# Optimization experiments

Hardware: AMD Instinct MI355X
Metric: run time of the kernel (lower is better)

The kernel has to match this reference:

```python
import jax, jax.numpy as jnp
import numpy as np

N = 20000   # nodes per type per hop
E = 200000  # edges per relation per hop
H = 512     # node_feature_hid_len
FU = 512    # raw user feature len
FI = 256    # raw item feature len
NUM_RES = 2
NUM_DNN = 2


def setup_inputs() -> dict:
    key = jax.random.key(0)
    ks = iter(jax.random.split(key, 64))
    p = lambda shape: jax.random.normal(next(ks), shape, dtype=jnp.float32) * 0.05
    inp = {}
    # features per hop per type
    for h in range(3):
        inp[f'feat_user_h{h}'] = jax.random.normal(next(ks), (N, FU), dtype=jnp.float32)
        inp[f'feat_item_h{h}'] = jax.random.normal(next(ks), (N, FI), dtype=jnp.float32)
    del inp['feat_user_h2_']; 


def _unused():
    pass

# rebuild setup_inputs cleanly (above stub replaced)

def setup_inputs() -> dict:
    key = jax.random.key(0)
    ks = iter(jax.random.split(key, 64))
    p = lambda shape: jax.random.normal(next(ks), shape, dtype=jnp.float32) * 0.05
    inp = {}
    for h in range(3):
        inp[f'feat_user_h{h}'] = jax.random.normal(next(ks), (N, FU), dtype=jnp.float32)
        inp[f'feat_item_h{h}'] = jax.random.normal(next(ks), (N, FI), dtype=jnp.float32)
    for name in ('edges_UI_h0', 'edges_IU_h0', 'edges_UI_h1', 'edges_IU_h1'):
        inp[name] = jax.random.randint(next(ks), (2, E), 0, N, dtype=jnp.int32)
    # per-node-type input transforms
    inp['W_user'] = p((FU, H)); inp['b_user'] = jnp.zeros((H,), jnp.float32)
    inp['W_item'] = p((FI, H)); inp['b_item'] = jnp.zeros((H,), jnp.float32)
    # per-relation GATConv params, stacked over 2 relations [UI, IU]
    inp['gat_feat_W'] = p((2, H, H)); inp['gat_feat_b'] = jnp.zeros((2, H), jnp.float32)
    inp['gat_att_w'] = p((2, 2 * H)); inp['gat_att_b'] = jnp.zeros((2,), jnp.float32)
    inp['gat_bias'] = jnp.zeros((2, H), jnp.float32)
    # Res_DNN params
    inp['prep_W'] = p((H, H)); inp['prep_b'] = jnp.zeros((H,), jnp.float32)
    inp['dnn_W'] = p((NUM_RES, NUM_DNN, H, H)); inp['dnn_b'] = jnp.zeros((NUM_RES, NUM_DNN, H), jnp.float32)
    inp['dnn_ln_g'] = jnp.ones((NUM_RES, NUM_DNN, H), jnp.float32); inp['dnn_ln_b'] = jnp.zeros((NUM_RES, NUM_DNN, H), jnp.float32)
    inp['res_ln_g'] = jnp.ones((NUM_RES, H), jnp.float32); inp['res_ln_b'] = jnp.zeros((NUM_RES, H), jnp.float32)
    inp['cls_W'] = p((H, 1)); inp['cls_b'] = jnp.zeros((1,), jnp.float32)
    return inp


def _ln(x, g, b, eps=1e-5):
    mu = jnp.mean(x, axis=-1, keepdims=True)
    var = jnp.mean((x - mu) ** 2, axis=-1, keepdims=True)
    return (x - mu) * jax.lax.rsqrt(var + eps) * g + b


def _gat(head_h, tail_h, edges, fW, fb, aw, ab, bias):
    # GATConv: feat_linear on both sides, tanh edge attention, per-source-row
    # sparse softmax, scatter-weighted sum of transformed tail features.
    s = head_h @ fW + fb            # [Nh, H]
    t = tail_h @ fW + fb            # [Nt, H]
    src, tgt = edges[0], edges[1]
    # att(cat([s_e, t_e])) split into per-node scores (same math as concat @ aw)
    e = jnp.tanh((s @ aw[:H])[src] + (t @ aw[H:])[tgt] + ab)  # [E]
    nh = head_h.shape[0]
    m = jax.ops.segment_max(e, src, num_segments=nh)
    ex = jnp.exp(e - m[src])
    den = jax.ops.segment_sum(ex, src, num_segments=nh)
    alpha = ex / den[src]
    hp = jax.ops.segment_sum(alpha[:, None] * t[tgt], src, num_segments=nh)
    return hp + bias


def _forward(feat_user_h0, feat_item_h0, feat_user_h1, feat_item_h1,
             feat_user_h2, feat_item_h2,
             W_user, b_user, W_item, b_item,
             gat_feat_W, gat_feat_b, gat_att_w, gat_att_b, gat_bias,
             prep_W, prep_b, dnn_W, dnn_b, dnn_ln_g, dnn_ln_b,
             res_ln_g, res_ln_b, cls_W, cls_b,
             edges_UI_h0, edges_IU_h0, edges_UI_h1, edges_IU_h1):
    def gat(r, head, tail, edges):
        return _gat(head, tail, edges, gat_feat_W[r], gat_feat_b[r],
                    gat_att_w[r], gat_att_b[r], gat_bias[r])
    # hop 2 (deepest): transformed source features
    su = feat_user_h2 @ W_user + b_user
    si = feat_item_h2 @ W_item + b_item
    # hop 1
    hu = feat_user_h1 @ W_user + b_user
    hi = feat_item_h1 @ W_item + b_item
    su_new = (hu + gat(0, hu, si, edges_UI_h1)) * 0.5  # mean of [self, UI agg]
    si_new = (hi + gat(1, hi, su, edges_IU_h1)) * 0.5
    su, si = su_new, si_new
    # hop 0
    hu = feat_user_h0 @ W_user + b_user
    hi = feat_item_h0 @ W_item + b_item
    su_new = (hu + gat(0, hu, si, edges_UI_h0)) * 0.5
    su = su_new  # target node type = 'user' (first key)
    # Res_DNN head
    x = su @ prep_W + prep_b
    for r in range(NUM_RES):
        sc = x
        for d in range(NUM_DNN):
            x = _ln(jnp.tanh(x @ dnn_W[r, d] + dnn_b[r, d]), dnn_ln_g[r, d], dnn_ln_b[r, d])
        x = _ln(jnp.tanh(sc + x), res_ln_g[r], res_ln_b[r])
    return jax.nn.sigmoid(x @ cls_W + cls_b)  # [N, 1]


def reference(feat_user_h0, feat_item_h0, feat_user_h1, feat_item_h1,
              feat_user_h2, feat_item_h2,
              edges_UI_h0, edges_IU_h0, edges_UI_h1, edges_IU_h1,
              W_user, b_user, W_item, b_item,
              gat_feat_W, gat_feat_b, gat_att_w, gat_att_b, gat_bias,
              prep_W, prep_b, dnn_W, dnn_b, dnn_ln_g, dnn_ln_b,
              res_ln_g, res_ln_b, cls_W, cls_b):
    return _forward(feat_user_h0, feat_item_h0, feat_user_h1, feat_item_h1,
                    feat_user_h2, feat_item_h2,
                    W_user, b_user, W_item, b_item,
                    gat_feat_W, gat_feat_b, gat_att_w, gat_att_b, gat_bias,
                    prep_W, prep_b, dnn_W, dnn_b, dnn_ln_g, dnn_ln_b,
                    res_ln_g, res_ln_b, cls_W, cls_b,
                    edges_UI_h0, edges_IU_h0, edges_UI_h1, edges_IU_h1)
```

## Files before the change

### kernel.cpp

```cpp
#include <hip/hip_runtime.h>
#include <math.h>

#define NN 20000
#define NE 200000
#define HH 512

typedef __attribute__((ext_vector_type(8))) short short8v;
typedef __attribute__((ext_vector_type(4))) float f32x4;

__device__ inline short f2bf(float f) {
    union { float f; unsigned u; } v; v.f = f;
    unsigned r = (v.u + 0x7fffu + ((v.u >> 16) & 1u)) >> 16;
    return (short)r;
}
__device__ inline float bf2f(short s) {
    union { unsigned u; float f; } v;
    v.u = ((unsigned)(unsigned short)s) << 16;
    return v.f;
}

__device__ inline void gload_lds16(const void* g, void* l) {
    __builtin_amdgcn_global_load_lds(
        (const __attribute__((address_space(1))) void*)g,
        (__attribute__((address_space(3))) void*)l, 16, 0, 0);
}

__global__ __launch_bounds__(256)
void wtr_all(const float* __restrict__ Wu, const float* __restrict__ Wi,
             const float* __restrict__ gfW, const float* __restrict__ prW,
             const float* __restrict__ dW,
             short* __restrict__ WTu, short* __restrict__ WTi,
             short* __restrict__ WTg0, short* __restrict__ WTg1,
             short* __restrict__ WTpr, short* __restrict__ WTd)
{
    __shared__ float t[32][33];
    int z = blockIdx.z;
    const float* src; short* dst; int K;
    if (z == 0)      { src = Wu;  dst = WTu;  K = 512; }
    else if (z == 1) { src = Wi;  dst = WTi;  K = 256; }
    else if (z == 2) { src = gfW; dst = WTg0; K = 512; }
    else if (z == 3) { src = gfW + (size_t)512 * 512; dst = WTg1; K = 512; }
    else if (z == 4) { src = prW; dst = WTpr; K = 512; }
    else { src = dW + (size_t)(z - 5) * 512 * 512;
           dst = WTd + (size_t)(z - 5) * 512 * 512; K = 512; }
    int by = blockIdx.y * 32;
    if (by >= K) return;
    int bx = blockIdx.x * 32;
    int tx = threadIdx.x, ty = threadIdx.y;
    for (int i = ty; i < 32; i += 8)
        t[i][tx] = src[(size_t)(by + i) * 512 + bx + tx];
    __syncthreads();
    for (int i = ty; i < 32; i += 8)
        dst[(size_t)(bx + i) * K + by + tx] = f2bf(t[tx][i]);
}

__global__ __launch_bounds__(256)
void mfma_lin(const short* __restrict__ X, const short* __restrict__ WT,
              const float* __restrict__ bias, float* __restrict__ outF,
              short* __restrict__ outB, int M, int K,
              const short* __restrict__ rdH, const short* __restrict__ rdT,
              const float* __restrict__ rduv, const float* __restrict__ rds0,
              float* __restrict__ rdss, float* __restrict__ rdts, int rdN)
{
    __shared__ short8v pool[4096];

    const int tid = threadIdx.x;
    const int lane = tid & 63;
    const int w = tid >> 6;

    const int nby = (M + 127) >> 7;
    const int nwg = nby << 2;
    int id = blockIdx.x;

    if (id >= nwg) {
        int row = (id - nwg) * 4 + w;
        if (row >= rdN) return;
        short8v h = ((const short8v*)(rdH + (size_t)row * HH))[lane];
        short8v t = ((const short8v*)(rdT + (size_t)row * HH))[lane];
        const float4* up = (const float4*)rduv + lane * 2;
        const float4* vp = (const float4*)(rduv + HH) + lane * 2;
        float4 u0 = up[0], u1 = up[1], v0 = vp[0], v1 = vp[1];
        float a = bf2f(h[0])*u0.x + bf2f(h[1])*u0.y + bf2f(h[2])*u0.z + bf2f(h[3])*u0.w
                + bf2f(h[4])*u1.x + bf2f(h[5])*u1.y + bf2f(h[6])*u1.z + bf2f(h[7])*u1.w;
        float b = bf2f(t[0])*v0.x + bf2f(t[1])*v0.y + bf2f(t[2])*v0.z + bf2f(t[3])*v0.w
                + bf2f(t[4])*v1.x + bf2f(t[5])*v1.y + bf2f(t[6])*v1.z + bf2f(t[7])*v1.w;
#pragma unroll
        for (int m = 32; m >= 1; m >>= 1) {
            a += __shfl_xor(a, m);
            b += __shfl_xor(b, m);
        }
        if (lane == 0) { rdss[row] = a + rds0[0]; rdts[row] = b + rds0[1]; }
        return;
    }

    const int q = nwg >> 3, r = nwg & 7;
    int xcd = id & 7, wi = id >> 3;
    int wgid = (xcd < r ? xcd * (q + 1) : r * (q + 1) + (xcd - r) * q) + wi;
    const int col0 = (wgid & 3) * 128;
    const int row0 = (wgid >> 2) * 128;

    const int wr = (w >> 1) * 64;
    const int wc = (w & 1) * 64;

    const short* gsrc[8];
#pragma unroll
    for (int g = 0; g < 8; ++g) {
        int p = w * 512 + g * 64 + lane;
        if (p < 1024) {
            int row = p >> 3;
            int c = (p & 7) ^ (row & 7);
            int ga = row0 + row; if (ga >= M) ga = M - 1;
            gsrc[g] = X + (size_t)ga * K + c * 8;
        } else {
            int qq = p - 1024;
            int col = qq >> 3;
            int c = (qq & 7) ^ (col & 7);
            gsrc[g] = WT + (size_t)(col0 + col) * K + c * 8;
        }
    }

    int ar[2][4], br[2][4];
#pragma unroll
    for (int kk = 0; kk < 2; ++kk) {
#pragma unroll
        for (int i = 0; i < 4; ++i) {
            int rr = wr + i * 16 + (lane & 15);
            ar[kk][i] = rr * 8 + ((kk * 4 + (lane >> 4)) ^ (rr & 7));
            int nn = wc + i * 16 + (lane & 15);
            br[kk][i] = 1024 + nn * 8 + ((kk * 4 + (lane >> 4)) ^ (nn & 7));
        }
    }

    f32x4 acc[4][4];
#pragma unroll
    for (int i = 0; i < 4; ++i)
#pragma unroll
        for (int j = 0; j < 4; ++j)
            acc[i][j] = (f32x4){0.f, 0.f, 0.f, 0.f};

    auto stage = [&](int buf, int kk) {
        short8v* base = pool + buf * 2048 + w * 512;
#pragma unroll
        for (int g = 0; g < 8; ++g)
            gload_lds16(gsrc[g] + kk, base + g * 64);
    };

    const int nt = K >> 6;
    stage(0, 0);
    if (nt > 1) stage(1, 64);
    int cur = 0;
    for (int t = 0; t < nt; ++t) {
        if (t + 1 < nt) asm volatile("s_waitcnt vmcnt(8)" ::: "memory");
        else            asm volatile("s_waitcnt vmcnt(0)" ::: "memory");
        __builtin_amdgcn_s_barrier();
        const short8v* S = pool + cur * 2048;
#pragma unroll
        for (int kk = 0; kk < 2; ++kk) {
            short8v af[4], bf[4];
#pragma unroll
            for (int i = 0; i < 4; ++i) af[i] = S[ar[kk][i]];
#pragma unroll
            for (int j = 0; j < 4; ++j) bf[j] = S[br[kk][j]];
#pragma unroll
            for (int i = 0; i < 4; ++i)
#pragma unroll
                for (int j = 0; j < 4; ++j)
                    acc[i][j] = __builtin_amdgcn_mfma_f32_16x16x32_bf16(af[i], bf[j], acc[i][j], 0, 0, 0);
        }
        __builtin_amdgcn_s_barrier();
        if (t + 2 < nt) stage(cur, (t + 2) * 64);
        cur ^= 1;
    }

    float bj[4];
#pragma unroll
    for (int j = 0; j < 4; ++j)
        bj[j] = bias[col0 + wc + j * 16 + (lane & 15)];

    if (outF) {
#pragma unroll
        for (int i = 0; i < 4; ++i) {
#pragma unroll
            for (int rr = 0; rr < 4; ++rr) {
                int row = row0 + wr + i * 16 + (lane >> 4) * 4 + rr;
                if (row < M) {
                    float* op = outF + (size_t)row * HH + col0 + wc + (lane & 15);
#pragma unroll
                    for (int j = 0; j < 4; ++j) op[j * 16] = acc[i][j][rr] + bj[j];
                }
            }
        }
    }
    if (outB) {
        short* lt = (short*)pool;
#pragma unroll
        for (int i = 0; i < 4; ++i)
#pragma unroll
            for (int rr = 0; rr < 4; ++rr) {
                int lrow = wr + i * 16 + (lane >> 4) * 4 + rr;
#pragma unroll
                for (int j = 0; j < 4; ++j)
                    lt[lrow * 136 + wc + j * 16 + (lane & 15)] = f2bf(acc[i][j][rr] + bj[j]);
            }
        __syncthreads();
#pragma unroll
        for (int k = 0; k < 8; ++k) {
            int row = (tid >> 4) + 16 * k;
            int seg = tid & 15;
            int grow = row0 + row;
            if (grow < M) {
                short8v vv = *(short8v*)(lt + row * 136 + seg * 8);
                *(short8v*)(outB + (size_t)grow * HH + col0 + seg * 8) = vv;
            }
        }
    }
}

__global__ __launch_bounds__(256)
void mfma_linf(const float* __restrict__ XA, const float* __restrict__ XB2,
               int NA, const short* __restrict__ WT,
               const float* __restrict__ bias, short* __restrict__ outB,
               int M, int K)
{
    __shared__ short8v pool[2304];

    const int tid = threadIdx.x;
    const int lane = tid & 63;
    const int w = tid >> 6;

    const int nby = (M + 127) >> 7;
    const int nwg = nby << 2;
    const int q = nwg >> 3, r = nwg & 7;
    int id = blockIdx.x;
    int xcd = id & 7, wi = id >> 3;
    int wgid = (xcd < r ? xcd * (q + 1) : r * (q + 1) + (xcd - r) * q) + wi;
    const int col0 = (wgid & 3) * 128;
    const int row0 = (wgid >> 2) * 128;

    const int wr = (w >> 1) * 64;
    const int wc = (w & 1) * 64;

    const int srow = tid >> 1;
    const int sc0 = (tid & 1) * 2;
    int garow = row0 + srow; if (garow >= M) garow = M - 1;
    const float* abase = ((garow < NA) ? XA + (size_t)garow * K
                                       : XB2 + (size_t)(garow - NA) * K) + sc0 * 8;
    const int aswz = (srow >> 1) & 3;
    const int wi0 = srow * 4 + (sc0 ^ aswz);
    const int wi1 = srow * 4 + ((sc0 + 1) ^ aswz);

    const short* bsrc0; const short* bsrc1;
    int bbase0, bbase1;
    {
        int p0 = w * 128 + lane;
        int col = p0 >> 2;
        int c = (p0 & 3) ^ ((col >> 1) & 3);
        bsrc0 = WT + (size_t)(col0 + col) * K + c * 8;
        bbase0 = w * 128;
        int p1 = w * 128 + 64 + lane;
        col = p1 >> 2;
        c = (p1 & 3) ^ ((col >> 1) & 3);
        bsrc1 = WT + (size_t)(col0 + col) * K + c * 8;
        bbase1 = w * 128 + 64;
    }

    int ar[4], br[4];
#pragma unroll
    for (int i = 0; i < 4; ++i) {
        int rr = wr + i * 16 + (lane & 15);
        ar[i] = rr * 4 + ((lane >> 4) ^ ((rr >> 1) & 3));
        int nn = wc + i * 16 + (lane & 15);
        br[i] = 512 + nn * 4 + ((lane >> 4) ^ ((nn >> 1) & 3));
    }

    f32x4 acc[4][4];
#pragma unroll
    for (int i = 0; i < 4; ++i)
#pragma unroll
        for (int j = 0; j < 4; ++j)
            acc[i][j] = (f32x4){0.f, 0.f, 0.f, 0.f};

    const int nt = K >> 5;
    float4 rA0[4], rA1[4];

#define ISSUE_A(RA, T) {                                                   \
        const float4* p_ = (const float4*)(abase + (T) * 32);              \
        RA[0] = p_[0]; RA[1] = p_[1]; RA[2] = p_[2]; RA[3] = p_[3]; }
#define ISSUE_B(BUF, T) {                                                  \
        short8v* bb_ = pool + (BUF) * 1024 + 512;                          \
        gload_lds16(bsrc0 + (T) * 32, bb_ + bbase0);                       \
        gload_lds16(bsrc1 + (T) * 32, bb_ + bbase1); }
#define LINF_BODY(BUF, RA, T) {                                            \
        short8v s0_, s1_;                                                  \
        s0_[0]=f2bf(RA[0].x); s0_[1]=f2bf(RA[0].y); s0_[2]=f2bf(RA[0].z); s0_[3]=f2bf(RA[0].w); \
        s0_[4]=f2bf(RA[1].x); s0_[5]=f2bf(RA[1].y); s0_[6]=f2bf(RA[1].z); s0_[7]=f2bf(RA[1].w); \
        s1_[0]=f2bf(RA[2].x); s1_[1]=f2bf(RA[2].y); s1_[2]=f2bf(RA[2].z); s1_[3]=f2bf(RA[2].w); \
        s1_[4]=f2bf(RA[3].x); s1_[5]=f2bf(RA[3].y); s1_[6]=f2bf(RA[3].z); s1_[7]=f2bf(RA[3].w); \
        short8v* A_ = pool + (BUF) * 1024;                                 \
        A_[wi0] = s0_; A_[wi1] = s1_;                                      \
        if ((T) + 1 < nt) asm volatile("s_waitcnt vmcnt(6) lgkmcnt(0)" ::: "memory"); \
        else              asm volatile("s_waitcnt vmcnt(0) lgkmcnt(0)" ::: "memory"); \
        __builtin_amdgcn_s_barrier();                                      \
        const short8v* S_ = pool + (BUF) * 1024;                           \
        short8v af_[4], bf_[4];                                            \
        _Pragma("unroll")                                                  \
        for (int i_ = 0; i_ < 4; ++i_) af_[i_] = S_[ar[i_]];               \
        _Pragma("unroll")                                                  \
        for (int j_ = 0; j_ < 4; ++j_) bf_[j_] = S_[br[j_]];               \
        _Pragma("unroll")                                                  \
        for (int i_ = 0; i_ < 4; ++i_)                                     \
            _Pragma("unroll")                                              \
            for (int j_ = 0; j_ < 4; ++j_)                                 \
                acc[i_][j_] = __builtin_amdgcn_mfma_f32_16x16x32_bf16(af_[i_], bf_[j_], acc[i_][j_], 0, 0, 0); \
        __builtin_amdgcn_s_barrier();                                      \
        if ((T) + 2 < nt) { ISSUE_A(RA, (T) + 2); ISSUE_B(BUF, (T) + 2); } }

    ISSUE_A(rA0, 0);
    ISSUE_B(0, 0);
    ISSUE_A(rA1, 1);
    ISSUE_B(1, 1);
    for (int t = 0; t < nt; t += 2) {
        LINF_BODY(0, rA0, t);
        LINF_BODY(1, rA1, t + 1);
    }
#undef ISSUE_A
#undef ISSUE_B
#undef LINF_BODY

    float bj[4];
#pragma unroll
    for (int j = 0; j < 4; ++j)
        bj[j] = bias[col0 + wc + j * 16 + (lane & 15)];

    short* lt = (short*)pool;
#pragma unroll
    for (int i = 0; i < 4; ++i)
#pragma unroll
        for (int rr = 0; rr < 4; ++rr) {
            int lrow = wr + i * 16 + (lane >> 4) * 4 + rr;
#pragma unroll
            for (int j = 0; j < 4; ++j)
                lt[lrow * 136 + wc + j * 16 + (lane & 15)] = f2bf(acc[i][j][rr] + bj[j]);
        }
    __syncthreads();
#pragma unroll
    for (int k = 0; k < 8; ++k) {
        int row = (tid >> 4) + 16 * k;
        int seg = tid & 15;
        int grow = row0 + row;
        if (grow < M) {
            short8v vv = *(short8v*)(lt + row * 136 + seg * 8);
            *(short8v*)(outB + (size_t)grow * HH + col0 + seg * 8) = vv;
        }
    }
}

__global__ __launch_bounds__(256)
void gat_pre2(const float* __restrict__ gfW, const float* __restrict__ gfb,
              const float* __restrict__ gaw, float* __restrict__ uvall,
              float* __restrict__ s0t0all)
{
    int rrel = blockIdx.y;
    const float* fW = gfW + (size_t)rrel * HH * HH;
    const float* fb = gfb + rrel * HH;
    const float* aw = gaw + (size_t)rrel * 2 * HH;
    float* uv = uvall + rrel * 1024;
    float* s0t0 = s0t0all + rrel * 4;
    int row = blockIdx.x * 4 + (threadIdx.x >> 6);
    int lane = threadIdx.x & 63;
    const float4* ah = (const float4*)aw;
    const float4* at = (const float4*)(aw + HH);
    const float4* fp;
    if (row < 512)       fp = (const float4*)(fW + (size_t)row * HH);
    else if (row == 512) fp = (const float4*)fb;
    else return;
    float du = 0.f, dv = 0.f;
#pragma unroll
    for (int l = 0; l < 2; ++l) {
        int idx = lane * 2 + l;
        float4 f = fp[idx], a = ah[idx], b = at[idx];
        du += f.x*a.x + f.y*a.y + f.z*a.z + f.w*a.w;
        dv += f.x*b.x + f.y*b.y + f.z*b.z + f.w*b.w;
    }
#pragma unroll
    for (int m = 32; m >= 1; m >>= 1) {
        du += __shfl_xor(du, m);
        dv += __shfl_xor(dv, m);
    }
    if (lane == 0) {
        if (row < 512) { uv[row] = du; uv[512 + row] = dv; }
        else           { s0t0[0] = du; s0t0[1] = dv; }
    }
}

__global__ __launch_bounds__(256)
void count2_kernel(const int* __restrict__ s0, const int* __restrict__ s1,
                   int* __restrict__ c0, int* __restrict__ c1, int E)
{
    int i = blockIdx.x * blockDim.x + threadIdx.x;
    if (i < E) atomicAdd(&c0[s0[i]], 1);
    else if (i < 2 * E) atomicAdd(&c1[s1[i - E]], 1);
}

__global__ __launch_bounds__(1024)
void scan2_kernel(const int* __restrict__ c0, const int* __restrict__ c1,
                  int* __restrict__ o0, int* __restrict__ o1,
                  int* __restrict__ u0, int* __restrict__ u1, int n)
{
    const int* counts = blockIdx.x ? c1 : c0;
    int* offs = blockIdx.x ? o1 : o0;
    int* curs = blockIdx.x ? u1 : u0;
    __shared__ int part[1024];
    const int tid = threadIdx.x;
    const int CH = (n + 1023) / 1024;
    const int base = tid * CH;
    int s = 0;
    for (int i = 0; i < CH; ++i) {
        int idx = base + i;
        if (idx < n) s += counts[idx];
    }
    part[tid] = s;
    __syncthreads();
    for (int d = 1; d < 1024; d <<= 1) {
        int v = 0;
        if (tid >= d) v = part[tid - d];
        __syncthreads();
        if (tid >= d) part[tid] += v;
        __syncthreads();
    }
    int run = (tid == 0) ? 0 : part[tid - 1];
    for (int i = 0; i < CH; ++i) {
        int idx = base + i;
        if (idx < n) { offs[idx] = run; curs[idx] = run; run += counts[idx]; }
    }
    if (tid == 1023) offs[n] = run;
}

__global__ __launch_bounds__(256)
void fill_kernel(const int* __restrict__ src, const int* __restrict__ tgt,
                 const float* __restrict__ ss, const float* __restrict__ ts,
                 const float* __restrict__ ab_ptr, int* __restrict__ cursor,
                 int* __restrict__ tvals, float* __restrict__ wv,
                 int* __restrict__ eidx, int E)
{
    int i = blockIdx.x * blockDim.x + threadIdx.x;
    if (i >= E) return;
    int s = src[i], t = tgt[i];
    int pos = atomicAdd(&cursor[s], 1);
    tvals[pos] = t;
    wv[pos] = expf(tanhf(ss[s] + ts[t] + ab_ptr[0]));
    eidx[pos] = i;
}

__global__ __launch_bounds__(256)
void gat_agg_kernel(const int* __restrict__ offs, const int* __restrict__ tvals,
                    const float* __restrict__ wv, const int* __restrict__ eidx,
                    const short* __restrict__ T, const short* __restrict__ head,
                    const float* __restrict__ gbias, short* __restrict__ out, int N)
{
    __shared__ int   slt[4][512];
    __shared__ float slw[4][512];
    int w = threadIdx.x >> 6;
    int lane = threadIdx.x & 63;
    int s = blockIdx.x * 4 + w;
    if (s >= N) return;
    const int beg = offs[s], end = offs[s + 1];
    int L = end - beg;
    if (L > 512) L = 512;

    if (L <= 64) {
        int e = 0x7fffffff, t = 0; float fw = 0.f;
        if (lane < L) { e = eidx[beg + lane]; t = tvals[beg + lane]; fw = wv[beg + lane]; }
        int r = 0;
        for (int k = 0; k < L; ++k)
            r += (__shfl(e, k) < e) ? 1 : 0;
        if (lane < L) { slt[w][r] = t; slw[w][r] = fw; }
    } else {
        for (int j = lane; j < L; j += 64) {
            int e = eidx[beg + j];
            int r = 0;
            for (int k = 0; k < L; ++k) r += (eidx[beg + k] < e) ? 1 : 0;
            slt[w][r] = tvals[beg + j]; slw[w][r] = wv[beg + j];
        }
    }
    asm volatile("s_waitcnt lgkmcnt(0)" ::: "memory");

    float a[8];
#pragma unroll
    for (int q = 0; q < 8; ++q) a[q] = 0.f;
    float den = 0.f;

    int j = 0;
    for (; j + 8 <= L; j += 8) {
        short8v v[8];
        float wgt[8];
#pragma unroll
        for (int u = 0; u < 8; ++u) {
            wgt[u] = slw[w][j + u];
            v[u] = ((const short8v*)(T + (size_t)slt[w][j + u] * HH))[lane];
        }
#pragma unroll
        for (int u = 0; u < 8; ++u) {
            den += wgt[u];
#pragma unroll
            for (int q = 0; q < 8; ++q) a[q] = fmaf(wgt[u], bf2f(v[u][q]), a[q]);
        }
    }
    for (; j + 4 <= L; j += 4) {
        short8v v[4];
        float wgt[4];
#pragma unroll
        for (int u = 0; u < 4; ++u) {
            wgt[u] = slw[w][j + u];
            v[u] = ((const short8v*)(T + (size_t)slt[w][j + u] * HH))[lane];
        }
#pragma unroll
        for (int u = 0; u < 4; ++u) {
            den += wgt[u];
#pragma unroll
            for (int q = 0; q < 8; ++q) a[q] = fmaf(wgt[u], bf2f(v[u][q]), a[q]);
        }
    }
    for (; j < L; ++j) {
        float fw = slw[w][j];
        short8v tv = ((const short8v*)(T + (size_t)slt[w][j] * HH))[lane];
        den += fw;
#pragma unroll
        for (int q = 0; q < 8; ++q) a[q] = fmaf(fw, bf2f(tv[q]), a[q]);
    }
    float inv = (den > 0.f) ? 1.f / den : 0.f;

    short8v h = ((const short8v*)(head + (size_t)s * HH))[lane];
    const float4* bp = (const float4*)gbias + lane * 2;
    float4 b0 = bp[0], b1 = bp[1];
    float bb[8] = {b0.x, b0.y, b0.z, b0.w, b1.x, b1.y, b1.z, b1.w};
    short8v o;
#pragma unroll
    for (int q = 0; q < 8; ++q)
        o[q] = f2bf((bf2f(h[q]) + a[q] * inv + bb[q]) * 0.5f);
    ((short8v*)(out + (size_t)s * HH))[lane] = o;
}

__global__ __launch_bounds__(256)
void tanh_ln_kernel(const short* __restrict__ Z,
                    const float* __restrict__ g, const float* __restrict__ bta,
                    short* __restrict__ outB, int N)
{
    int row = blockIdx.x * 4 + (threadIdx.x >> 6);
    int lane = threadIdx.x & 63;
    if (row >= N) return;
    short8v zv = ((const short8v*)(Z + (size_t)row * HH))[lane];
    float v[8];
    float sum = 0.f, sum2 = 0.f;
#pragma unroll
    for (int q = 0; q < 8; ++q) {
        float t = tanhf(bf2f(zv[q]));
        v[q] = t; sum += t; sum2 = fmaf(t, t, sum2);
    }
#pragma unroll
    for (int m = 32; m >= 1; m >>= 1) {
        sum += __shfl_xor(sum, m); sum2 += __shfl_xor(sum2, m);
    }
    float mu = sum * (1.f/HH);
    float rs = rsqrtf(sum2 * (1.f/HH) - mu*mu + 1e-5f);
    const float4* gp = (const float4*)g + lane * 2;
    const float4* bp = (const float4*)bta + lane * 2;
    float4 g0 = gp[0], g1 = gp[1], c0 = bp[0], c1 = bp[1];
    float gg[8] = {g0.x, g0.y, g0.z, g0.w, g1.x, g1.y, g1.z, g1.w};
    float cc[8] = {c0.x, c0.y, c0.z, c0.w, c1.x, c1.y, c1.z, c1.w};
    short8v ob;
#pragma unroll
    for (int q = 0; q < 8; ++q) ob[q] = f2bf((v[q]-mu)*rs*gg[q] + cc[q]);
    ((short8v*)(outB + (size_t)row * HH))[lane] = ob;
}

__global__ __launch_bounds__(256)
void tanh_ln2_kernel(const short* __restrict__ Z, const float* __restrict__ sc,
                     const float* __restrict__ g1, const float* __restrict__ b1,
                     const float* __restrict__ g2, const float* __restrict__ b2,
                     short* __restrict__ outB, float* __restrict__ outF,
                     const float* __restrict__ cWp, const float* __restrict__ cbp,
                     float* __restrict__ outCls, int N)
{
    int row = blockIdx.x * 4 + (threadIdx.x >> 6);
    int lane = threadIdx.x & 63;
    if (row >= N) return;
    short8v zv = ((const short8v*)(Z + (size_t)row * HH))[lane];
    float v[8];
    float sum = 0.f, sum2 = 0.f;
#pragma unroll
    for (int q = 0; q < 8; ++q) {
        float t = tanhf(bf2f(zv[q]));
        v[q] = t; sum += t; sum2 = fmaf(t, t, sum2);
    }
#pragma unroll
    for (int m = 32; m >= 1; m >>= 1) {
        sum += __shfl_xor(sum, m); sum2 += __shfl_xor(sum2, m);
    }
    float mu = sum * (1.f/HH);
    float rs = rsqrtf(sum2 * (1.f/HH) - mu*mu + 1e-5f);
    {
        const float4* gp = (const float4*)g1 + lane * 2;
        const float4* bp = (const float4*)b1 + lane * 2;
        float4 g0 = gp[0], g1v = gp[1], c0 = bp[0], c1 = bp[1];
        float gg[8] = {g0.x, g0.y, g0.z, g0.w, g1v.x, g1v.y, g1v.z, g1v.w};
        float cc[8] = {c0.x, c0.y, c0.z, c0.w, c1.x, c1.y, c1.z, c1.w};
        const float4* sp = (const float4*)(sc + (size_t)row * HH) + lane * 2;
        float4 s0 = sp[0], s1 = sp[1];
        float ssv[8] = {s0.x, s0.y, s0.z, s0.w, s1.x, s1.y, s1.z, s1.w};
        sum = 0.f; sum2 = 0.f;
#pragma unroll
        for (int q = 0; q < 8; ++q) {
            float x2 = (v[q]-mu)*rs*gg[q] + cc[q];
            float t = tanhf(ssv[q] + x2);
            v[q] = t; sum += t; sum2 = fmaf(t, t, sum2);
        }
    }
#pragma unroll
    for (int m = 32; m >= 1; m >>= 1) {
        sum += __shfl_xor(sum, m); sum2 += __shfl_xor(sum2, m);
    }
    mu = sum * (1.f/HH);
    rs = rsqrtf(sum2 * (1.f/HH) - mu*mu + 1e-5f);
    const float4* gp = (const float4*)g2 + lane * 2;
    const float4* bp = (const float4*)b2 + lane * 2;
    float4 g0 = gp[0], g1v = gp[1], c0 = bp[0], c1 = bp[1];
    float gg[8] = {g0.x, g0.y, g0.z, g0.w, g1v.x, g1v.y, g1v.z, g1v.w};
    float cc[8] = {c0.x, c0.y, c0.z, c0.w, c1.x, c1.y, c1.z, c1.w};
    float o[8];
#pragma unroll
    for (int q = 0; q < 8; ++q) o[q] = (v[q]-mu)*rs*gg[q] + cc[q];
    if (outB) {
        short8v ob;
#pragma unroll
        for (int q = 0; q < 8; ++q) ob[q] = f2bf(o[q]);
        ((short8v*)(outB + (size_t)row * HH))[lane] = ob;
    }
    if (outF) {
        float4* op = (float4*)(outF + (size_t)row * HH) + lane * 2;
        op[0] = make_float4(o[0], o[1], o[2], o[3]);
        op[1] = make_float4(o[4], o[5], o[6], o[7]);
    }
    if (cWp) {
        const float4* wp = (const float4*)cWp + lane * 2;
        float4 w0 = wp[0], w1 = wp[1];
        float acc = o[0]*w0.x + o[1]*w0.y + o[2]*w0.z + o[3]*w0.w
                  + o[4]*w1.x + o[5]*w1.y + o[6]*w1.z + o[7]*w1.w;
#pragma unroll
        for (int m = 32; m >= 1; m >>= 1) acc += __shfl_xor(acc, m);
        if (lane == 0) outCls[row] = 1.f / (1.f + expf(-(acc + cbp[0])));
    }
}

extern "C" void kernel_launch(void* const* d_in, const int* in_sizes, int n_in,
                              void* d_out, int out_size, void* d_ws, size_t ws_size,
                              hipStream_t stream)
{
    (void)in_sizes; (void)n_in; (void)out_size; (void)ws_size;
    const int N = NN, E = NE, H = HH;
    const size_t NHf = (size_t)N * H;

    const float* fu0 = (const float*)d_in[0];
    const float* fi1 = (const float*)d_in[3];
    const float* fu2 = (const float*)d_in[4];
    const int* eUI0 = (const int*)d_in[6];
    const int* eIU1 = (const int*)d_in[9];
    const float* Wu  = (const float*)d_in[10];
    const float* bu  = (const float*)d_in[11];
    const float* Wi  = (const float*)d_in[12];
    const float* bi  = (const float*)d_in[13];
    const float* gfW = (const float*)d_in[14];
    const float* gfb = (const float*)d_in[15];
    const float* gaw = (const float*)d_in[16];
    const float* gab = (const float*)d_in[17];
    const float* gbias = (const float*)d_in[18];
    const float* prW = (const float*)d_in[19];
    const float* prb = (const float*)d_in[20];
    const float* dW  = (const float*)d_in[21];
    const float* db  = (const float*)d_in[22];
    const float* dlg = (const float*)d_in[23];
    const float* dlb = (const float*)d_in[24];
    const float* rlg = (const float*)d_in[25];
    const float* rlb = (const float*)d_in[26];
    const float* cW  = (const float*)d_in[27];
    const float* cb  = (const float*)d_in[28];

    float* B5     = (float*)d_ws;
    float* ssb    = B5 + NHf;
    float* tsb    = ssb + N;
    float* uvall  = tsb + N;
    float* s0t0a  = uvall + 2048;
    float* wvb    = s0t0a + 8;
    int* counts0 = (int*)(wvb + E);
    int* counts1 = counts0 + N;
    int* offs0   = counts1 + N;
    int* offs1   = offs0 + N + 1;
    int* cur0    = offs1 + N + 1;
    int* cur1    = cur0 + N;
    int* tvals   = cur1 + N;
    int* eidxb   = tvals + E;
    size_t boff = (size_t)((char*)(eidxb + E) - (char*)d_ws);
    boff = (boff + 15) & ~(size_t)15;
    short* SUHU  = (short*)((char*)d_ws + boff);
    short* HI    = SUHU + 2 * NHf;
    short* SINEW = HI + NHf;
    short* T4    = SINEW + NHf;
    short* SUF   = T4 + NHf;
    short* WTu   = SUF + NHf;
    short* WTi   = WTu + 512 * 512;
    short* WTg0  = WTi + 512 * 256;
    short* WTg1  = WTg0 + 512 * 512;
    short* WTpr  = WTg1 + 512 * 512;
    short* WTd   = WTpr + 512 * 512;
    short* SU  = SUHU;
    short* HU0 = SUHU + NHf;
    short* XB  = SINEW;
    short* ZB  = SU;

    hipLaunchKernelGGL(wtr_all, dim3(16, 16, 9), dim3(32, 8), 0, stream,
                       Wu, Wi, gfW, prW, dW, WTu, WTi, WTg0, WTg1, WTpr, WTd);
    hipMemsetAsync(counts0, 0, 2 * N * sizeof(int), stream);
    hipLaunchKernelGGL(count2_kernel, dim3((2 * E + 255) / 256), dim3(256), 0, stream,
                       eUI0, eIU1, counts0, counts1, E);
    hipLaunchKernelGGL(scan2_kernel, dim3(2), dim3(1024), 0, stream,
                       counts0, counts1, offs0, offs1, cur0, cur1, N);
    hipLaunchKernelGGL(gat_pre2, dim3(130, 2), dim3(256), 0, stream,
                       gfW, gfb, gaw, uvall, s0t0a);

    const int rgrid = (N + 3) / 4;
    const int egrid = (E + 255) / 256;
    auto MLIN = [&](const short* X, const short* WT, const float* b,
                    float* oF, short* oB, int M, int K,
                    const short* rdH, const short* rdT, const float* rduv,
                    const float* rds0) {
        int nwg = ((M + 127) / 128) * 4;
        int grid = nwg + (rdH ? rgrid : 0);
        hipLaunchKernelGGL(mfma_lin, dim3(grid), dim3(256), 0, stream,
                           X, WT, b, oF, oB, M, K,
                           rdH, rdT, rduv, rds0, ssb, tsb, N);
    };
    auto MLINF = [&](const float* XA, const float* XB2, int NA, const short* WT,
                     const float* b, short* oB, int M, int K) {
        int nwg = ((M + 127) / 128) * 4;
        hipLaunchKernelGGL(mfma_linf, dim3(nwg), dim3(256), 0, stream,
                           XA, XB2, NA, WT, b, oB, M, K);
    };

    auto GAT = [&](int r, const short* headB, const short* tailB, const short* WTg,
                   const int* edges, int* offs, int* curs, short* outB) {
        MLIN(tailB, WTg, gfb + r * H, nullptr, T4, N, 512,
             headB, tailB, uvall + r * 1024, s0t0a + r * 4);
        hipLaunchKernelGGL(fill_kernel, dim3(egrid), dim3(256), 0, stream,
                           edges, edges + E, ssb, tsb, gab + r, curs, tvals, wvb,
                           eidxb, E);
        hipLaunchKernelGGL(gat_agg_kernel, dim3(rgrid), dim3(256), 0, stream,
                           offs, tvals, wvb, eidxb, T4, headB,
                           gbias + (size_t)r * H, outB, N);
    };

    MLINF(fu2, fu0, N, WTu, bu, SUHU, 2 * N, 512);
    MLINF(fi1, fi1, N, WTi, bi, HI, N, 256);
    GAT(1, HI, SU, WTg1, eIU1, offs1, cur1, SINEW);
    GAT(0, HU0, SINEW, WTg0, eUI0, offs0, cur0, SUF);

    MLIN(SUF, WTpr, prb, B5, XB, N, 512, nullptr, nullptr, nullptr, nullptr);
    for (int r = 0; r < 2; ++r) {
        MLIN(XB, WTd + (size_t)(r * 2) * 512 * 512, db + (r * 2) * H,
             nullptr, ZB, N, 512, nullptr, nullptr, nullptr, nullptr);
        hipLaunchKernelGGL(tanh_ln_kernel, dim3(rgrid), dim3(256), 0, stream,
                           ZB, dlg + (r * 2) * H, dlb + (r * 2) * H, XB, N);
        MLIN(XB, WTd + (size_t)(r * 2 + 1) * 512 * 512, db + (r * 2 + 1) * H,
             nullptr, ZB, N, 512, nullptr, nullptr, nullptr, nullptr);
        if (r == 0) {
            hipLaunchKernelGGL(tanh_ln2_kernel, dim3(rgrid), dim3(256), 0, stream,
                               ZB, B5, dlg + H, dlb + H, rlg, rlb,
                               XB, B5, (const float*)nullptr, (const float*)nullptr,
                               (float*)nullptr, N);
        } else {
            hipLaunchKernelGGL(tanh_ln2_kernel, dim3(rgrid), dim3(256), 0, stream,
                               ZB, B5, dlg + 3 * H, dlb + 3 * H, rlg + H, rlb + H,
                               (short*)nullptr, (float*)nullptr, cW, cb,
                               (float*)d_out, N);
        }
    }
}
```

Baseline: 503.0 us.

## Fold user input transform into first GAT feature weight to skip intermediate GEMM

```diff
diff --git a/kernel.cpp b/kernel.cpp
--- a/kernel.cpp
+++ b/kernel.cpp
@@ -31,10 +31,20 @@
              const float* __restrict__ dW,
              short* __restrict__ WTu, short* __restrict__ WTi,
              short* __restrict__ WTg0, short* __restrict__ WTg1,
-             short* __restrict__ WTpr, short* __restrict__ WTd)
+             short* __restrict__ WTpr, short* __restrict__ WTd,
+             short* __restrict__ WuB)
 {
     __shared__ float t[32][33];
     int z = blockIdx.z;
+    int by = blockIdx.y * 32;
+    int bx = blockIdx.x * 32;
+    int tx = threadIdx.x, ty = threadIdx.y;
+    if (z == 9) {
+        for (int i = ty; i < 32; i += 8)
+            WuB[(size_t)(by + i) * 512 + bx + tx] =
+                f2bf(Wu[(size_t)(by + i) * 512 + bx + tx]);
+        return;
+    }
     const float* src; short* dst; int K;
     if (z == 0)      { src = Wu;  dst = WTu;  K = 512; }
     else if (z == 1) { src = Wi;  dst = WTi;  K = 256; }
@@ -43,10 +53,7 @@
     else if (z == 4) { src = prW; dst = WTpr; K = 512; }
     else { src = dW + (size_t)(z - 5) * 512 * 512;
            dst = WTd + (size_t)(z - 5) * 512 * 512; K = 512; }
-    int by = blockIdx.y * 32;
     if (by >= K) return;
-    int bx = blockIdx.x * 32;
-    int tx = threadIdx.x, ty = threadIdx.y;
     for (int i = ty; i < 32; i += 8)
         t[i][tx] = src[(size_t)(by + i) * 512 + bx + tx];
     __syncthreads();
@@ -74,7 +81,7 @@
 
     if (id >= nwg) {
         int row = (id - nwg) * 4 + w;
-        if (row >= rdN) return;
+        if (!rdH || row >= rdN) return;
         short8v h = ((const short8v*)(rdH + (size_t)row * HH))[lane];
         short8v t = ((const short8v*)(rdT + (size_t)row * HH))[lane];
         const float4* up = (const float4*)rduv + lane * 2;
@@ -175,7 +182,7 @@
     float bj[4];
 #pragma unroll
     for (int j = 0; j < 4; ++j)
-        bj[j] = bias[col0 + wc + j * 16 + (lane & 15)];
+        bj[j] = bias ? bias[col0 + wc + j * 16 + (lane & 15)] : 0.f;
 
     if (outF) {
 #pragma unroll
@@ -220,7 +227,11 @@
 void mfma_linf(const float* __restrict__ XA, const float* __restrict__ XB2,
                int NA, const short* __restrict__ WT,
                const float* __restrict__ bias, short* __restrict__ outB,
-               int M, int K)
+               int M, int K,
+               const short* __restrict__ rdH, const float* __restrict__ rdT32,
+               const float* __restrict__ rdu, const float* __restrict__ rdwuv,
+               const float* __restrict__ rdc, float* __restrict__ rdss,
+               float* __restrict__ rdts, int rdN)
 {
     __shared__ short8v pool[2304];
 
@@ -230,8 +241,31 @@
 
     const int nby = (M + 127) >> 7;
     const int nwg = nby << 2;
+    int id = blockIdx.x;
+
+    if (id >= nwg) {
+        int row = (id - nwg) * 4 + w;
+        if (!rdH || row >= rdN) return;
+        short8v h = ((const short8v*)(rdH + (size_t)row * HH))[lane];
+        const float4* tp = (const float4*)(rdT32 + (size_t)row * HH) + lane * 2;
+        float4 t0v = tp[0], t1v = tp[1];
+        const float4* up = (const float4*)rdu + lane * 2;
+        const float4* vp = (const float4*)rdwuv + lane * 2;
+        float4 u0 = up[0], u1 = up[1], v0 = vp[0], v1 = vp[1];
+        float a = bf2f(h[0])*u0.x + bf2f(h[1])*u0.y + bf2f(h[2])*u0.z + bf2f(h[3])*u0.w
+                + bf2f(h[4])*u1.x + bf2f(h[5])*u1.y + bf2f(h[6])*u1.z + bf2f(h[7])*u1.w;
+        float b = t0v.x*v0.x + t0v.y*v0.y + t0v.z*v0.z + t0v.w*v0.w
+                + t1v.x*v1.x + t1v.y*v1.y + t1v.z*v1.z + t1v.w*v1.w;
+#pragma unroll
+        for (int m = 32; m >= 1; m >>= 1) {
+            a += __shfl_xor(a, m);
+            b += __shfl_xor(b, m);
+        }
+        if (lane == 0) { rdss[row] = a + rdc[0]; rdts[row] = b + rdc[1]; }
+        return;
+    }
+
     const int q = nwg >> 3, r = nwg & 7;
-    int id = blockIdx.x;
     int xcd = id & 7, wi = id >> 3;
     int wgid = (xcd < r ? xcd * (q + 1) : r * (q + 1) + (xcd - r) * q) + wi;
     const int col0 = (wgid & 3) * 128;
@@ -394,6 +428,46 @@
 }
 
 __global__ __launch_bounds__(256)
+void wuvbc_kernel(const float* __restrict__ Wu, const float* __restrict__ bu,
+                  const short* __restrict__ WTg1, const float* __restrict__ fb1,
+                  const float* __restrict__ uvall, const float* __restrict__ s0t0a,
+                  float* __restrict__ wuv, float* __restrict__ cpair,
+                  float* __restrict__ bcomp)
+{
+    int row = blockIdx.x * 4 + (threadIdx.x >> 6);
+    int lane = threadIdx.x & 63;
+    if (blockIdx.y == 0) {
+        const float* v1 = uvall + 1024 + 512;
+        const float4* vp = (const float4*)v1 + lane * 2;
+        float4 v0 = vp[0], v1v = vp[1];
+        const float4* fp;
+        if (row < 512)       fp = (const float4*)(Wu + (size_t)row * HH);
+        else if (row == 512) fp = (const float4*)bu;
+        else return;
+        const float4* p = fp + lane * 2;
+        float4 a = p[0], b = p[1];
+        float d = a.x*v0.x + a.y*v0.y + a.z*v0.z + a.w*v0.w
+                + b.x*v1v.x + b.y*v1v.y + b.z*v1v.z + b.w*v1v.w;
+#pragma unroll
+        for (int m = 32; m >= 1; m >>= 1) d += __shfl_xor(d, m);
+        if (lane == 0) {
+            if (row < 512) wuv[row] = d;
+            else { cpair[0] = s0t0a[4]; cpair[1] = d + s0t0a[5]; }
+        }
+    } else {
+        if (row >= 512) return;
+        short8v wv8 = ((const short8v*)(WTg1 + (size_t)row * HH))[lane];
+        const float4* bp = (const float4*)bu + lane * 2;
+        float4 b0 = bp[0], b1 = bp[1];
+        float d = bf2f(wv8[0])*b0.x + bf2f(wv8[1])*b0.y + bf2f(wv8[2])*b0.z + bf2f(wv8[3])*b0.w
+                + bf2f(wv8[4])*b1.x + bf2f(wv8[5])*b1.y + bf2f(wv8[6])*b1.z + bf2f(wv8[7])*b1.w;
+#pragma unroll
+        for (int m = 32; m >= 1; m >>= 1) d += __shfl_xor(d, m);
+        if (lane == 0) bcomp[row] = d + fb1[row];
+    }
+}
+
+__global__ __launch_bounds__(256)
 void count2_kernel(const int* __restrict__ s0, const int* __restrict__ s1,
                    int* __restrict__ c0, int* __restrict__ c1, int E)
 {
@@ -690,7 +764,10 @@
     float* tsb    = ssb + N;
     float* uvall  = tsb + N;
     float* s0t0a  = uvall + 2048;
-    float* wvb    = s0t0a + 8;
+    float* bcomp  = s0t0a + 8;
+    float* wuv    = bcomp + 512;
+    float* cpair  = wuv + 512;
+    float* wvb    = cpair + 4;
     int* counts0 = (int*)(wvb + E);
     int* counts1 = counts0 + N;
     int* offs0   = counts1 + N;
@@ -701,24 +778,25 @@
     int* eidxb   = tvals + E;
     size_t boff = (size_t)((char*)(eidxb + E) - (char*)d_ws);
     boff = (boff + 15) & ~(size_t)15;
-    short* SUHU  = (short*)((char*)d_ws + boff);
-    short* HI    = SUHU + 2 * NHf;
+    short* HU0   = (short*)((char*)d_ws + boff);
+    short* HI    = HU0 + NHf;
     short* SINEW = HI + NHf;
     short* T4    = SINEW + NHf;
     short* SUF   = T4 + NHf;
-    short* WTu   = SUF + NHf;
+    short* ZBUF  = SUF + NHf;
+    short* WTu   = ZBUF + NHf;
     short* WTi   = WTu + 512 * 512;
     short* WTg0  = WTi + 512 * 256;
     short* WTg1  = WTg0 + 512 * 512;
     short* WTpr  = WTg1 + 512 * 512;
     short* WTd   = WTpr + 512 * 512;
-    short* SU  = SUHU;
-    short* HU0 = SUHU + NHf;
+    short* WuB   = WTd + 4 * 512 * 512;
+    short* WTcmp = WuB + 512 * 512;
     short* XB  = SINEW;
-    short* ZB  = SU;
-
-    hipLaunchKernelGGL(wtr_all, dim3(16, 16, 9), dim3(32, 8), 0, stream,
-                       Wu, Wi, gfW, prW, dW, WTu, WTi, WTg0, WTg1, WTpr, WTd);
+    short* ZB  = ZBUF;
+
+    hipLaunchKernelGGL(wtr_all, dim3(16, 16, 10), dim3(32, 8), 0, stream,
+                       Wu, Wi, gfW, prW, dW, WTu, WTi, WTg0, WTg1, WTpr, WTd, WuB);
     hipMemsetAsync(counts0, 0, 2 * N * sizeof(int), stream);
     hipLaunchKernelGGL(count2_kernel, dim3((2 * E + 255) / 256), dim3(256), 0, stream,
                        eUI0, eIU1, counts0, counts1, E);
@@ -726,6 +804,13 @@
                        counts0, counts1, offs0, offs1, cur0, cur1, N);
     hipLaunchKernelGGL(gat_pre2, dim3(130, 2), dim3(256), 0, stream,
                        gfW, gfb, gaw, uvall, s0t0a);
+    hipLaunchKernelGGL(wuvbc_kernel, dim3(130, 2), dim3(256), 0, stream,
+                       Wu, bu, WTg1, gfb + H, uvall, s0t0a, wuv, cpair, bcomp);
+    hipLaunchKernelGGL(mfma_lin, dim3(16), dim3(256), 0, stream,
+                       WTg1, WuB, (const float*)nullptr, (float*)nullptr, WTcmp,
+                       512, 512, (const short*)nullptr, (const short*)nullptr,
+                       (const float*)nullptr, (const float*)nullptr,
+                       ssb, tsb, 0);
 
     const int rgrid = (N + 3) / 4;
     const int egrid = (E + 255) / 256;
@@ -739,29 +824,35 @@
                            X, WT, b, oF, oB, M, K,
                            rdH, rdT, rduv, rds0, ssb, tsb, N);
     };
-    auto MLINF = [&](const float* XA, const float* XB2, int NA, const short* WT,
-                     const float* b, short* oB, int M, int K) {
+    auto MLINF = [&](const float* XA, const short* WT, const float* b,
+                     short* oB, int M, int K,
+                     const short* rdH, const float* rdT32, const float* rdu,
+                     const float* rdwuv, const float* rdc) {
         int nwg = ((M + 127) / 128) * 4;
-        hipLaunchKernelGGL(mfma_linf, dim3(nwg), dim3(256), 0, stream,
-                           XA, XB2, NA, WT, b, oB, M, K);
+        int grid = nwg + (rdH ? rgrid : 0);
+        hipLaunchKernelGGL(mfma_linf, dim3(grid), dim3(256), 0, stream,
+                           XA, XA, M, WT, b, oB, M, K,
+                           rdH, rdT32, rdu, rdwuv, rdc, ssb, tsb, N);
     };
 
-    auto GAT = [&](int r, const short* headB, const short* tailB, const short* WTg,
-                   const int* edges, int* offs, int* curs, short* outB) {
-        MLIN(tailB, WTg, gfb + r * H, nullptr, T4, N, 512,
-             headB, tailB, uvall + r * 1024, s0t0a + r * 4);
-        hipLaunchKernelGGL(fill_kernel, dim3(egrid), dim3(256), 0, stream,
-                           edges, edges + E, ssb, tsb, gab + r, curs, tvals, wvb,
-                           eidxb, E);
-        hipLaunchKernelGGL(gat_agg_kernel, dim3(rgrid), dim3(256), 0, stream,
-                           offs, tvals, wvb, eidxb, T4, headB,
-                           gbias + (size_t)r * H, outB, N);
-    };
-
-    MLINF(fu2, fu0, N, WTu, bu, SUHU, 2 * N, 512);
-    MLINF(fi1, fi1, N, WTi, bi, HI, N, 256);
-    GAT(1, HI, SU, WTg1, eIU1, offs1, cur1, SINEW);
-    GAT(0, HU0, SINEW, WTg0, eUI0, offs0, cur0, SUF);
+    MLINF(fu0, WTu, bu, HU0, N, 512, nullptr, nullptr, nullptr, nullptr, nullptr);
+    MLINF(fi1, WTi, bi, HI, N, 256, nullptr, nullptr, nullptr, nullptr, nullptr);
+
+    MLINF(fu2, WTcmp, bcomp, T4, N, 512,
+          HI, fu2, uvall + 1024, wuv, cpair);
+    hipLaunchKernelGGL(fill_kernel, dim3(egrid), dim3(256), 0, stream,
+                       eIU1, eIU1 + E, ssb, tsb, gab + 1, cur1, tvals, wvb,
+                       eidxb, E);
+    hipLaunchKernelGGL(gat_agg_kernel, dim3(rgrid), dim3(256), 0, stream,
+                       offs1, tvals, wvb, eidxb, T4, HI, gbias + H, SINEW, N);
+
+    MLIN(SINEW, WTg0, gfb, nullptr, T4, N, 512,
+         HU0, SINEW, uvall, s0t0a);
+    hipLaunchKernelGGL(fill_kernel, dim3(egrid), dim3(256), 0, stream,
+                       eUI0, eUI0 + E, ssb, tsb, gab, cur0, tvals, wvb,
+                       eidxb, E);
+    hipLaunchKernelGGL(gat_agg_kernel, dim3(rgrid), dim3(256), 0, stream,
+                       offs0, tvals, wvb, eidxb, T4, HU0, gbias, SUF, N);
 
     MLIN(SUF, WTpr, prb, B5, XB, N, 512, nullptr, nullptr, nullptr, nullptr);
     for (int r = 0; r < 2; ++r) {
```

After: 496.7 us. About the same (-1.2%).
